# Kernel tuning notes

Measured on AMD Instinct MI355X. Metric: run time of the kernel, lower is better.

## Reference

```python
import jax, jax.numpy as jnp
import numpy as np

B, D, H = 4096, 1024, 1024


def setup_inputs() -> dict:
    key = jax.random.key(0)
    ks = jax.random.split(key, 20)
    s_in = 1.0 / np.sqrt(D)
    s_hid = 1.0 / np.sqrt(H)
    inp = {
        "x_t": jax.random.normal(ks[0], (B, D), dtype=jnp.float32),
        "h_t_1": jax.random.normal(ks[1], (B, H), dtype=jnp.float32),
        "c_t_1": jax.random.normal(ks[2], (B, H), dtype=jnp.float32),
        # input-to-hidden weights (nn.Linear: y = x @ W.T + b), stacked i,f,o,z
        "W": jax.random.uniform(ks[3], (4, H, D), minval=-s_in, maxval=s_in, dtype=jnp.float32),
        "bW": jax.random.uniform(ks[4], (4, H), minval=-s_in, maxval=s_in, dtype=jnp.float32),
        # hidden-to-hidden weights, stacked i,f,o,z
        "U": jax.random.uniform(ks[5], (4, H, H), minval=-s_hid, maxval=s_hid, dtype=jnp.float32),
        "bU": jax.random.uniform(ks[6], (4, H), minval=-s_hid, maxval=s_hid, dtype=jnp.float32),
    }
    return inp


def reference(x_t, h_t_1, c_t_1, W, bW, U, bU):
    # Two stacked GEMMs: [B,D]x[4,H,D] -> [4,B,H], [B,H]x[4,H,H] -> [4,B,H]
    gx = jnp.einsum("bd,ghd->gbh", x_t, W) + bW[:, None, :]
    gh = jnp.einsum("bh,gkh->gbk", h_t_1, U) + bU[:, None, :]
    g = gx + gh  # [4, B, H] pre-activations for i, f, o, z
    i = jax.nn.sigmoid(g[0])
    f = jax.nn.sigmoid(g[1])
    o = jax.nn.sigmoid(g[2])
    z = jnp.tanh(g[3])
    c_t = i * z + f * c_t_1
    h_t = o * jnp.tanh(c_t)
    return (h_t, c_t)
```

## Files before the change

kernel.cpp:

```cpp
#include <hip/hip_runtime.h>
#include <math.h>

#define Mm 4096
#define Nn 4096
#define Kk 2048

typedef __bf16 bf16x8 __attribute__((ext_vector_type(8)));
typedef float f32x4 __attribute__((ext_vector_type(4)));

__device__ __forceinline__ unsigned short f2bf(float f) {
    union { float f; unsigned u; } v; v.f = f;
    unsigned r = v.u + 0x7FFFu + ((v.u >> 16) & 1u);
    return (unsigned short)(r >> 16);
}

__device__ __forceinline__ float fast_tanh(float x) {
    return 1.f - 2.f / (1.f + __expf(2.f * x));
}

__global__ void pack_bf16(const float* __restrict__ x, const float* __restrict__ h,
                          const float* __restrict__ W, const float* __restrict__ U,
                          const float* __restrict__ bW, const float* __restrict__ bU,
                          unsigned short* __restrict__ Xc, unsigned short* __restrict__ Wc,
                          float* __restrict__ bsum) {
    if (blockIdx.x == 0) {
#pragma unroll
        for (int j = 0; j < 16; ++j) {
            int n = threadIdx.x * 16 + j;
            int hh = n >> 2, g = n & 3;
            bsum[n] = bW[g * 1024 + hh] + bU[g * 1024 + hh];
        }
    }
    const int PER = (4096 * 1024) / 4;
    for (int t = blockIdx.x * blockDim.x + threadIdx.x; t < 4 * PER;
         t += gridDim.x * blockDim.x) {
        int region = t >> 20;
        int i = t & (PER - 1);
        int row = i >> 8;
        int c4  = i & 255;
        const float* src = (region == 0) ? x : (region == 1) ? h : (region == 2) ? W : U;
        float4 v = reinterpret_cast<const float4*>(src)[i];
        ushort4 o;
        o.x = f2bf(v.x); o.y = f2bf(v.y); o.z = f2bf(v.z); o.w = f2bf(v.w);
        if (region < 2) {
            *reinterpret_cast<ushort4*>(Xc + (size_t)row * 2048 + (region << 10) + c4 * 4) = o;
        } else {
            int g = row >> 10, hh = row & 1023;
            int np = ((hh >> 4) << 6) + (g << 4) + (hh & 15);
            *reinterpret_cast<ushort4*>(Wc + (size_t)np * 2048 + ((region & 1) << 10) + c4 * 4) = o;
        }
    }
}

__device__ __forceinline__ void gl16(const void* g, void* l) {
    __builtin_amdgcn_global_load_lds(
        (const __attribute__((address_space(1))) void*)g,
        (__attribute__((address_space(3))) void*)l, 16, 0, 0);
}

#define A_OFF(p, ah) (((p) * 2 + (ah)) * 16384)
#define B_OFF(p, hb) (65536 + ((p) * 2 + (hb)) * 16384)

__global__ __launch_bounds__(512, 2) void gemm_8ph(const unsigned short* __restrict__ A,
                                                   const unsigned short* __restrict__ Bw,
                                                   const float* __restrict__ bsum,
                                                   const float* __restrict__ cprev,
                                                   float* __restrict__ out) {
    extern __shared__ char lds[];
    const int tid = threadIdx.x, lane = tid & 63, wave = tid >> 6;
    const int wm = wave >> 2, wn = wave & 3;

    const int bid = blockIdx.x;
    const int swz = (bid & 7) * 32 + (bid >> 3);
    const int bm = swz & 15, bn = swz >> 4;
    const size_t Crow0 = (size_t)bm * 256, Ccol0 = (size_t)bn * 256;

    const int srow = wave * 8 + (lane >> 3);
    const int scolswz = (((lane & 7) ^ (lane >> 3)) << 4);
    const char* aS[2][2];
    const char* bS[2][2];
#pragma unroll
    for (int ah = 0; ah < 2; ++ah)
#pragma unroll
        for (int j = 0; j < 2; ++j) {
            aS[ah][j] = (const char*)A  + (size_t)(Crow0 + ah * 128 + j * 64 + srow) * 4096 + scolswz;
            bS[ah][j] = (const char*)Bw + (size_t)(Ccol0 + ah * 128 + j * 64 + srow) * 4096 + scolswz;
        }

#define STG_A(p, ah, kb) do { \
        gl16(aS[ah][0] + (kb), lds + A_OFF(p, ah) + wave * 1024); \
        gl16(aS[ah][1] + (kb), lds + A_OFF(p, ah) + 8192 + wave * 1024); } while (0)
#define STG_B(p, hb, kb) do { \
        gl16(bS[hb][0] + (kb), lds + B_OFF(p, hb) + wave * 1024); \
        gl16(bS[hb][1] + (kb), lds + B_OFF(p, hb) + 8192 + wave * 1024); } while (0)

    const int arowB = (wm * 64 + (lane & 15)) * 128;
    const int browB = ((wn & 1) * 64 + (lane & 15)) * 128;
    const int c0 = (((lane >> 4) << 4)) ^ ((lane & 7) << 4);
    const int c1 = (64 + ((lane >> 4) << 4)) ^ ((lane & 7) << 4);
    const int bhb = wn >> 1;

#define LDA(p, ah, mfl, ck) (*(const bf16x8*)(lds + A_OFF(p, ah) + arowB + (mfl) * 2048 + (ck)))
#define LDB(p, nf, ck)      (*(const bf16x8*)(lds + B_OFF(p, bhb) + browB + (nf) * 2048 + (ck)))

    f32x4 acc[2][4][4] = {};

#define MFMA(a, b, c) __builtin_amdgcn_mfma_f32_16x16x32_bf16(a, b, c, 0, 0, 0)
#define MF16(ah, mfA, mfB, p00, p01, p10, p11) \
    acc[ah][mfA][0] = MFMA(p00, b00, acc[ah][mfA][0]); \
    acc[ah][mfA][1] = MFMA(p00, b10, acc[ah][mfA][1]); \
    acc[ah][mfA][2] = MFMA(p00, b20, acc[ah][mfA][2]); \
    acc[ah][mfA][3] = MFMA(p00, b30, acc[ah][mfA][3]); \
    acc[ah][mfB][0] = MFMA(p10, b00, acc[ah][mfB][0]); \
    acc[ah][mfB][1] = MFMA(p10, b10, acc[ah][mfB][1]); \
    acc[ah][mfB][2] = MFMA(p10, b20, acc[ah][mfB][2]); \
    acc[ah][mfB][3] = MFMA(p10, b30, acc[ah][mfB][3]); \
    acc[ah][mfA][0] = MFMA(p01, b01, acc[ah][mfA][0]); \
    acc[ah][mfA][1] = MFMA(p01, b11, acc[ah][mfA][1]); \
    acc[ah][mfA][2] = MFMA(p01, b21, acc[ah][mfA][2]); \
    acc[ah][mfA][3] = MFMA(p01, b31, acc[ah][mfA][3]); \
    acc[ah][mfB][0] = MFMA(p11, b01, acc[ah][mfB][0]); \
    acc[ah][mfB][1] = MFMA(p11, b11, acc[ah][mfB][1]); \
    acc[ah][mfB][2] = MFMA(p11, b21, acc[ah][mfB][2]); \
    acc[ah][mfB][3] = MFMA(p11, b31, acc[ah][mfB][3]);

#define SGB0 __builtin_amdgcn_sched_barrier(0)
#define SBAR __builtin_amdgcn_s_barrier()

#define GROUP(p, kbA1, kbT2) \
    { \
         \
        bf16x8 b00 = LDB(p, 0, c0), b01 = LDB(p, 0, c1), b10 = LDB(p, 1, c0), b11 = LDB(p, 1, c1); \
        bf16x8 b20 = LDB(p, 2, c0), b21 = LDB(p, 2, c1), b30 = LDB(p, 3, c0), b31 = LDB(p, 3, c1); \
        bf16x8 a0 = LDA(p, 0, 0, c0), a1 = LDA(p, 0, 0, c1); \
        bf16x8 a2 = LDA(p, 0, 1, c0), a3 = LDA(p, 0, 1, c1); \
        bf16x8 n0 = LDA(p, 0, 2, c0), n1 = LDA(p, 0, 2, c1); \
        bf16x8 n2 = LDA(p, 0, 3, c0), n3 = LDA(p, 0, 3, c1); \
        asm volatile("s_waitcnt vmcnt(6)" ::: "memory"); \
        SGB0; \
        __builtin_amdgcn_s_setprio(1); \
        MF16(0, 0, 1, a0, a1, a2, a3) \
        __builtin_amdgcn_s_setprio(0); \
        STG_A((p) ^ 1, 1, kbA1); \
        SBAR; \
         \
        a0 = LDA(p, 1, 0, c0); a1 = LDA(p, 1, 0, c1); \
        a2 = LDA(p, 1, 1, c0); a3 = LDA(p, 1, 1, c1); \
        asm volatile("s_waitcnt vmcnt(6)" ::: "memory"); \
        SGB0; \
        __builtin_amdgcn_s_setprio(1); \
        MF16(0, 2, 3, n0, n1, n2, n3) \
        __builtin_amdgcn_s_setprio(0); \
        STG_B(p, 0, kbT2); \
        SBAR; \
         \
        n0 = LDA(p, 1, 2, c0); n1 = LDA(p, 1, 2, c1); \
        n2 = LDA(p, 1, 3, c0); n3 = LDA(p, 1, 3, c1); \
        asm volatile("s_waitcnt vmcnt(6)" ::: "memory"); \
        SGB0; \
        __builtin_amdgcn_s_setprio(1); \
        MF16(1, 0, 1, a0, a1, a2, a3) \
        __builtin_amdgcn_s_setprio(0); \
        STG_A(p, 0, kbT2); \
        SBAR; \
         \
        SGB0; \
        __builtin_amdgcn_s_setprio(1); \
        MF16(1, 2, 3, n0, n1, n2, n3) \
        __builtin_amdgcn_s_setprio(0); \
        STG_B(p, 1, kbT2); \
        SBAR; \
    }

    STG_B(0, 0, 0);
    STG_A(0, 0, 0);
    STG_B(0, 1, 0);
    STG_A(0, 1, 0);
    STG_B(1, 0, 128);
    STG_A(1, 0, 128);
    STG_B(1, 1, 128);
    asm volatile("s_waitcnt vmcnt(6)" ::: "memory");
    __builtin_amdgcn_s_barrier();

    for (int it = 0; it < 16; ++it) {
        const int t0 = 2 * it;
        const size_t kA1_0 = (size_t)(t0 + 1) * 128;
        const size_t kT2_0 = (t0 + 2 <= 31) ? (size_t)(t0 + 2) * 128 : 0;
        const size_t kA1_1 = kT2_0;
        const size_t kT2_1 = (t0 + 3 <= 31) ? (size_t)(t0 + 3) * 128 : 0;
        GROUP(0, kA1_0, kT2_0)
        GROUP(1, kA1_1, kT2_1)
    }

    const int hl = lane & 15;
    const int er0 = (lane >> 4) * 4;
    const int myh = (int)(Ccol0 >> 2) + wn * 16 + hl;
    const f32x4 bs = *(const f32x4*)(bsum + (size_t)myh * 4);

    float cp[2][4][4];
#pragma unroll
    for (int ah = 0; ah < 2; ++ah)
#pragma unroll
        for (int mf = 0; mf < 4; ++mf)
#pragma unroll
            for (int r = 0; r < 4; ++r)
                cp[ah][mf][r] = cprev[(size_t)(Crow0 + ah * 128 + wm * 64 + mf * 16 + er0 + r) * 1024 + myh];

#pragma unroll
    for (int ah = 0; ah < 2; ++ah)
#pragma unroll
        for (int mf = 0; mf < 4; ++mf)
#pragma unroll
            for (int r = 0; r < 4; ++r) {
                float gi = acc[ah][mf][0][r] + bs[0];
                float gf = acc[ah][mf][1][r] + bs[1];
                float go = acc[ah][mf][2][r] + bs[2];
                float gz = acc[ah][mf][3][r] + bs[3];
                float iv = 1.f / (1.f + __expf(-gi));
                float fv = 1.f / (1.f + __expf(-gf));
                float ov = 1.f / (1.f + __expf(-go));
                float zv = fast_tanh(gz);
                float cc = fmaf(iv, zv, fv * cp[ah][mf][r]);
                float hv = ov * fast_tanh(cc);
                const size_t oidx =
                    (size_t)(Crow0 + ah * 128 + wm * 64 + mf * 16 + er0 + r) * 1024 + myh;
                out[oidx] = hv;
                out[(1 << 22) + oidx] = cc;
            }

    asm volatile("s_waitcnt vmcnt(0)" ::: "memory");
}

extern "C" void kernel_launch(void* const* d_in, const int* in_sizes, int n_in,
                              void* d_out, int out_size, void* d_ws, size_t ws_size,
                              hipStream_t stream) {
    const float* x  = (const float*)d_in[0];
    const float* h  = (const float*)d_in[1];
    const float* c  = (const float*)d_in[2];
    const float* W  = (const float*)d_in[3];
    const float* bW = (const float*)d_in[4];
    const float* U  = (const float*)d_in[5];
    const float* bU = (const float*)d_in[6];
    float* out = (float*)d_out;

    char* ws = (char*)d_ws;
    unsigned short* Xc = (unsigned short*)ws;
    unsigned short* Wc = (unsigned short*)(ws + ((size_t)16 << 20));
    float* bsum = (float*)(ws + ((size_t)32 << 20));

    (void)hipFuncSetAttribute((const void*)gemm_8ph,
                              hipFuncAttributeMaxDynamicSharedMemorySize, 131072);

    hipLaunchKernelGGL(pack_bf16, dim3(2048), dim3(256), 0, stream,
                       x, h, W, U, bW, bU, Xc, Wc, bsum);
    hipLaunchKernelGGL(gemm_8ph, dim3(256), dim3(512), 131072, stream,
                       Xc, Wc, bsum, c, out);
}
```

Baseline: 83.60 us.

## Restructure GEMM main loop into two 32-MFMA clusters with register prefetch

Reorganizes each k-step group from four 16-MFMA phases with four barriers into two 32-MFMA clusters with two barriers. The A fragments for the next stage's first half are loaded from LDS into registers ahead of time, so LDS reads overlap the MFMAs instead of waiting on them. Global staging pointers are now computed from a single base plus constant offsets, which saves address registers. The cost is higher VGPR pressure from 24 live bf16x8 operands and changed vmcnt wait points, which may hurt occupancy under the launch bounds or introduce ordering hazards.

```diff
diff --git a/kernel.cpp b/kernel.cpp
--- a/kernel.cpp
+++ b/kernel.cpp
@@ -77,22 +77,15 @@
 
     const int srow = wave * 8 + (lane >> 3);
     const int scolswz = (((lane & 7) ^ (lane >> 3)) << 4);
-    const char* aS[2][2];
-    const char* bS[2][2];
-#pragma unroll
-    for (int ah = 0; ah < 2; ++ah)
-#pragma unroll
-        for (int j = 0; j < 2; ++j) {
-            aS[ah][j] = (const char*)A  + (size_t)(Crow0 + ah * 128 + j * 64 + srow) * 4096 + scolswz;
-            bS[ah][j] = (const char*)Bw + (size_t)(Ccol0 + ah * 128 + j * 64 + srow) * 4096 + scolswz;
-        }
+    const char* aBase = (const char*)A  + (size_t)(Crow0 + srow) * 4096 + scolswz;
+    const char* bBase = (const char*)Bw + (size_t)(Ccol0 + srow) * 4096 + scolswz;
 
 #define STG_A(p, ah, kb) do { \
-        gl16(aS[ah][0] + (kb), lds + A_OFF(p, ah) + wave * 1024); \
-        gl16(aS[ah][1] + (kb), lds + A_OFF(p, ah) + 8192 + wave * 1024); } while (0)
+        gl16(aBase + (size_t)(ah) * 524288 + (kb),          lds + A_OFF(p, ah) + wave * 1024); \
+        gl16(aBase + (size_t)(ah) * 524288 + 262144 + (kb), lds + A_OFF(p, ah) + 8192 + wave * 1024); } while (0)
 #define STG_B(p, hb, kb) do { \
-        gl16(bS[hb][0] + (kb), lds + B_OFF(p, hb) + wave * 1024); \
-        gl16(bS[hb][1] + (kb), lds + B_OFF(p, hb) + 8192 + wave * 1024); } while (0)
+        gl16(bBase + (size_t)(hb) * 524288 + (kb),          lds + B_OFF(p, hb) + wave * 1024); \
+        gl16(bBase + (size_t)(hb) * 524288 + 262144 + (kb), lds + B_OFF(p, hb) + 8192 + wave * 1024); } while (0)
 
     const int arowB = (wm * 64 + (lane & 15)) * 128;
     const int browB = ((wn & 1) * 64 + (lane & 15)) * 128;
@@ -104,25 +97,44 @@
 #define LDB(p, nf, ck)      (*(const bf16x8*)(lds + B_OFF(p, bhb) + browB + (nf) * 2048 + (ck)))
 
     f32x4 acc[2][4][4] = {};
+    bf16x8 bb0, bb1, bb2, bb3, bb4, bb5, bb6, bb7;
+    bf16x8 aa0, aa1, aa2, aa3, aa4, aa5, aa6, aa7;
+    bf16x8 ab0, ab1, ab2, ab3, ab4, ab5, ab6, ab7;
 
 #define MFMA(a, b, c) __builtin_amdgcn_mfma_f32_16x16x32_bf16(a, b, c, 0, 0, 0)
-#define MF16(ah, mfA, mfB, p00, p01, p10, p11) \
-    acc[ah][mfA][0] = MFMA(p00, b00, acc[ah][mfA][0]); \
-    acc[ah][mfA][1] = MFMA(p00, b10, acc[ah][mfA][1]); \
-    acc[ah][mfA][2] = MFMA(p00, b20, acc[ah][mfA][2]); \
-    acc[ah][mfA][3] = MFMA(p00, b30, acc[ah][mfA][3]); \
-    acc[ah][mfB][0] = MFMA(p10, b00, acc[ah][mfB][0]); \
-    acc[ah][mfB][1] = MFMA(p10, b10, acc[ah][mfB][1]); \
-    acc[ah][mfB][2] = MFMA(p10, b20, acc[ah][mfB][2]); \
-    acc[ah][mfB][3] = MFMA(p10, b30, acc[ah][mfB][3]); \
-    acc[ah][mfA][0] = MFMA(p01, b01, acc[ah][mfA][0]); \
-    acc[ah][mfA][1] = MFMA(p01, b11, acc[ah][mfA][1]); \
-    acc[ah][mfA][2] = MFMA(p01, b21, acc[ah][mfA][2]); \
-    acc[ah][mfA][3] = MFMA(p01, b31, acc[ah][mfA][3]); \
-    acc[ah][mfB][0] = MFMA(p11, b01, acc[ah][mfB][0]); \
-    acc[ah][mfB][1] = MFMA(p11, b11, acc[ah][mfB][1]); \
-    acc[ah][mfB][2] = MFMA(p11, b21, acc[ah][mfB][2]); \
-    acc[ah][mfB][3] = MFMA(p11, b31, acc[ah][mfB][3]);
+#define CL32(ah, A0_, A1_, A2_, A3_, A4_, A5_, A6_, A7_) \
+    acc[ah][0][0] = MFMA(A0_, bb0, acc[ah][0][0]); \
+    acc[ah][0][1] = MFMA(A0_, bb2, acc[ah][0][1]); \
+    acc[ah][0][2] = MFMA(A0_, bb4, acc[ah][0][2]); \
+    acc[ah][0][3] = MFMA(A0_, bb6, acc[ah][0][3]); \
+    acc[ah][1][0] = MFMA(A2_, bb0, acc[ah][1][0]); \
+    acc[ah][1][1] = MFMA(A2_, bb2, acc[ah][1][1]); \
+    acc[ah][1][2] = MFMA(A2_, bb4, acc[ah][1][2]); \
+    acc[ah][1][3] = MFMA(A2_, bb6, acc[ah][1][3]); \
+    acc[ah][2][0] = MFMA(A4_, bb0, acc[ah][2][0]); \
+    acc[ah][2][1] = MFMA(A4_, bb2, acc[ah][2][1]); \
+    acc[ah][2][2] = MFMA(A4_, bb4, acc[ah][2][2]); \
+    acc[ah][2][3] = MFMA(A4_, bb6, acc[ah][2][3]); \
+    acc[ah][3][0] = MFMA(A6_, bb0, acc[ah][3][0]); \
+    acc[ah][3][1] = MFMA(A6_, bb2, acc[ah][3][1]); \
+    acc[ah][3][2] = MFMA(A6_, bb4, acc[ah][3][2]); \
+    acc[ah][3][3] = MFMA(A6_, bb6, acc[ah][3][3]); \
+    acc[ah][0][0] = MFMA(A1_, bb1, acc[ah][0][0]); \
+    acc[ah][0][1] = MFMA(A1_, bb3, acc[ah][0][1]); \
+    acc[ah][0][2] = MFMA(A1_, bb5, acc[ah][0][2]); \
+    acc[ah][0][3] = MFMA(A1_, bb7, acc[ah][0][3]); \
+    acc[ah][1][0] = MFMA(A3_, bb1, acc[ah][1][0]); \
+    acc[ah][1][1] = MFMA(A3_, bb3, acc[ah][1][1]); \
+    acc[ah][1][2] = MFMA(A3_, bb5, acc[ah][1][2]); \
+    acc[ah][1][3] = MFMA(A3_, bb7, acc[ah][1][3]); \
+    acc[ah][2][0] = MFMA(A5_, bb1, acc[ah][2][0]); \
+    acc[ah][2][1] = MFMA(A5_, bb3, acc[ah][2][1]); \
+    acc[ah][2][2] = MFMA(A5_, bb5, acc[ah][2][2]); \
+    acc[ah][2][3] = MFMA(A5_, bb7, acc[ah][2][3]); \
+    acc[ah][3][0] = MFMA(A7_, bb1, acc[ah][3][0]); \
+    acc[ah][3][1] = MFMA(A7_, bb3, acc[ah][3][1]); \
+    acc[ah][3][2] = MFMA(A7_, bb5, acc[ah][3][2]); \
+    acc[ah][3][3] = MFMA(A7_, bb7, acc[ah][3][3]);
 
 #define SGB0 __builtin_amdgcn_sched_barrier(0)
 #define SBAR __builtin_amdgcn_s_barrier()
@@ -130,57 +142,44 @@
 #define GROUP(p, kbA1, kbT2) \
     { \
          \
-        bf16x8 b00 = LDB(p, 0, c0), b01 = LDB(p, 0, c1), b10 = LDB(p, 1, c0), b11 = LDB(p, 1, c1); \
-        bf16x8 b20 = LDB(p, 2, c0), b21 = LDB(p, 2, c1), b30 = LDB(p, 3, c0), b31 = LDB(p, 3, c1); \
-        bf16x8 a0 = LDA(p, 0, 0, c0), a1 = LDA(p, 0, 0, c1); \
-        bf16x8 a2 = LDA(p, 0, 1, c0), a3 = LDA(p, 0, 1, c1); \
-        bf16x8 n0 = LDA(p, 0, 2, c0), n1 = LDA(p, 0, 2, c1); \
-        bf16x8 n2 = LDA(p, 0, 3, c0), n3 = LDA(p, 0, 3, c1); \
-        asm volatile("s_waitcnt vmcnt(6)" ::: "memory"); \
+        bb0 = LDB(p, 0, c0); bb1 = LDB(p, 0, c1); bb2 = LDB(p, 1, c0); bb3 = LDB(p, 1, c1); \
+        bb4 = LDB(p, 2, c0); bb5 = LDB(p, 2, c1); bb6 = LDB(p, 3, c0); bb7 = LDB(p, 3, c1); \
+        ab0 = LDA(p, 1, 0, c0); ab1 = LDA(p, 1, 0, c1); ab2 = LDA(p, 1, 1, c0); ab3 = LDA(p, 1, 1, c1); \
+        ab4 = LDA(p, 1, 2, c0); ab5 = LDA(p, 1, 2, c1); ab6 = LDA(p, 1, 3, c0); ab7 = LDA(p, 1, 3, c1); \
         SGB0; \
         __builtin_amdgcn_s_setprio(1); \
-        MF16(0, 0, 1, a0, a1, a2, a3) \
+        CL32(0, aa0, aa1, aa2, aa3, aa4, aa5, aa6, aa7) \
         __builtin_amdgcn_s_setprio(0); \
         STG_A((p) ^ 1, 1, kbA1); \
+        asm volatile("s_waitcnt vmcnt(2)" ::: "memory"); \
         SBAR; \
          \
-        a0 = LDA(p, 1, 0, c0); a1 = LDA(p, 1, 0, c1); \
-        a2 = LDA(p, 1, 1, c0); a3 = LDA(p, 1, 1, c1); \
-        asm volatile("s_waitcnt vmcnt(6)" ::: "memory"); \
+        aa0 = LDA((p) ^ 1, 0, 0, c0); aa1 = LDA((p) ^ 1, 0, 0, c1); \
+        aa2 = LDA((p) ^ 1, 0, 1, c0); aa3 = LDA((p) ^ 1, 0, 1, c1); \
+        aa4 = LDA((p) ^ 1, 0, 2, c0); aa5 = LDA((p) ^ 1, 0, 2, c1); \
+        aa6 = LDA((p) ^ 1, 0, 3, c0); aa7 = LDA((p) ^ 1, 0, 3, c1); \
         SGB0; \
         __builtin_amdgcn_s_setprio(1); \
-        MF16(0, 2, 3, n0, n1, n2, n3) \
-        __builtin_amdgcn_s_setprio(0); \
-        STG_B(p, 0, kbT2); \
-        SBAR; \
-         \
-        n0 = LDA(p, 1, 2, c0); n1 = LDA(p, 1, 2, c1); \
-        n2 = LDA(p, 1, 3, c0); n3 = LDA(p, 1, 3, c1); \
-        asm volatile("s_waitcnt vmcnt(6)" ::: "memory"); \
-        SGB0; \
-        __builtin_amdgcn_s_setprio(1); \
-        MF16(1, 0, 1, a0, a1, a2, a3) \
+        CL32(1, ab0, ab1, ab2, ab3, ab4, ab5, ab6, ab7) \
         __builtin_amdgcn_s_setprio(0); \
         STG_A(p, 0, kbT2); \
+        STG_B(p, 0, kbT2); \
+        STG_B(p, 1, kbT2); \
+        asm volatile("s_waitcnt vmcnt(6)" ::: "memory"); \
         SBAR; \
-         \
-        SGB0; \
-        __builtin_amdgcn_s_setprio(1); \
-        MF16(1, 2, 3, n0, n1, n2, n3) \
-        __builtin_amdgcn_s_setprio(0); \
-        STG_B(p, 1, kbT2); \
-        SBAR; \
-    }
-
-    STG_B(0, 0, 0);
+    }
+
     STG_A(0, 0, 0);
-    STG_B(0, 1, 0);
+    STG_B(0, 0, 0); STG_B(0, 1, 0);
     STG_A(0, 1, 0);
-    STG_B(1, 0, 128);
+    asm volatile("s_waitcnt vmcnt(0)" ::: "memory");
+    __builtin_amdgcn_s_barrier();
+    aa0 = LDA(0, 0, 0, c0); aa1 = LDA(0, 0, 0, c1);
+    aa2 = LDA(0, 0, 1, c0); aa3 = LDA(0, 0, 1, c1);
+    aa4 = LDA(0, 0, 2, c0); aa5 = LDA(0, 0, 2, c1);
+    aa6 = LDA(0, 0, 3, c0); aa7 = LDA(0, 0, 3, c1);
     STG_A(1, 0, 128);
-    STG_B(1, 1, 128);
-    asm volatile("s_waitcnt vmcnt(6)" ::: "memory");
-    __builtin_amdgcn_s_barrier();
+    STG_B(1, 0, 128); STG_B(1, 1, 128);
 
     for (int it = 0; it < 16; ++it) {
         const int t0 = 2 * it;
```

Result: slower. 87.34 us (+4.5%).
